# Optimization experiments

Hardware: AMD Instinct MI355X
Metric: run time of the kernel (lower is better)

## Reference

```python
import jax, jax.numpy as jnp
import numpy as np


def setup_inputs() -> dict:
    key = jax.random.key(0)
    k1, k2, k3 = jax.random.split(key, 3)
    B, L, S, H, E, D = 2, 512, 512, 8, 32, 64
    queries = jax.random.normal(k1, (B, L, H, E), dtype=jnp.float32)
    keys = jax.random.normal(k2, (B, S, H, E), dtype=jnp.float32)
    values = jax.random.normal(k3, (B, S, H, D), dtype=jnp.float32)
    v = jnp.ones((E,), dtype=jnp.float32)
    attn_mask_add = jnp.zeros((L, S), dtype=jnp.float32)
    key_lengths_add = jnp.zeros((B, S), dtype=jnp.float32)
    return {
        "queries": queries,
        "keys": keys,
        "values": values,
        "v": v,
        "attn_mask_add": attn_mask_add,
        "key_lengths_add": key_lengths_add,
    }


def reference(queries, keys, values, v, attn_mask_add, key_lengths_add):
    # Additive (Bahdanau) attention.
    # queries: (B,L,H,E), keys: (B,S,H,E), values: (B,S,H,D)
    # Broadcast add -> tanh -> contract with v: (B,L,S,H,E) -> (B,H,L,S)
    feat = jnp.tanh(queries[:, :, None, :, :] + keys[:, None, :, :, :])  # (B,L,S,H,E)
    scores = jnp.einsum("blshe,e->bhls", feat, v)  # (B,H,L,S)
    scores = scores + attn_mask_add[None, None, :, :]          # (L,S) attn mask
    scores = scores + key_lengths_add[:, None, None, :]        # (B,S) key-length mask
    A = jax.nn.softmax(scores, axis=-1)  # (B,H,L,S); dropout is identity (p=0 / eval)
    V = jnp.einsum("bhls,bshd->blhd", A, values)  # (B,L,H,D)
    return V
```

## Files before the change

kernel.cpp:

```cpp
#include <hip/hip_runtime.h>


#define BB 2
#define LL 512
#define SS 512
#define HH 8
#define EE 32
#define DD 64
#define TS 128
#define SASTR (SS + 8)

typedef __attribute__((ext_vector_type(8))) short bf16x8;
typedef __attribute__((ext_vector_type(4))) float f32x4;

__device__ __forceinline__ short f2bf(float f) {
    unsigned u = __float_as_uint(f);
    u += 0x7FFFu + ((u >> 16) & 1u);
    return (short)(u >> 16);
}

__device__ __forceinline__ float fast_exp2(float x) {
#if __has_builtin(__builtin_amdgcn_exp2f)
    return __builtin_amdgcn_exp2f(x);
#else
    return exp2f(x);
#endif
}
__device__ __forceinline__ float fast_rcp(float x) {
    return __builtin_amdgcn_rcpf(x);
}

__global__ __launch_bounds__(256) void addattn_kernel(
    const float* __restrict__ q,
    const float* __restrict__ k,
    const float* __restrict__ vals,
    const float* __restrict__ vvec,
    const float* __restrict__ mask,
    const float* __restrict__ klen,
    float* __restrict__ out)
{
    __shared__ float4 sk[EE / 4][TS];
    __shared__ short  sAb[4][SASTR];

    const int tid  = threadIdx.x;
    const int w    = tid >> 6;
    const int lane = tid & 63;
    const int bh   = blockIdx.x >> 7;
    const int lblk = blockIdx.x & 127;
    const int b    = bh >> 3;
    const int h    = bh & 7;
    const int l    = lblk * 4 + w;

    const float SC = 2.885390081777927f;

    float4 eq[EE / 4];
    {
        const float4* qrow = (const float4*)(q + (((size_t)b * LL + l) * HH + h) * EE);
        #pragma unroll
        for (int e4 = 0; e4 < EE / 4; e4++) {
            float4 t = qrow[e4];
            eq[e4] = make_float4(fast_exp2(SC * t.x), fast_exp2(SC * t.y),
                                 fast_exp2(SC * t.z), fast_exp2(SC * t.w));
        }
    }
    float4 v2[EE / 4];
    {
        const float4* vr = (const float4*)vvec;
        #pragma unroll
        for (int i = 0; i < EE / 4; i++) {
            float4 t = vr[i];
            v2[i] = make_float4(-2.f * t.x, -2.f * t.y, -2.f * t.z, -2.f * t.w);
        }
    }

    float sc[SS / 64];
    const float4* krow = (const float4*)(k + ((size_t)b * SS * HH + h) * EE);
    for (int t = 0; t < SS / TS; t++) {
        __syncthreads();
        #pragma unroll
        for (int i = 0; i < (TS * (EE / 4)) / 256; i++) {
            int idx = tid + i * 256;
            int ss  = idx >> 3;
            int e4  = idx & 7;
            float4 kv = krow[(size_t)(t * TS + ss) * (HH * EE / 4) + e4];
            sk[e4][ss ^ e4] = make_float4(
                fast_exp2(SC * kv.x), fast_exp2(SC * kv.y),
                fast_exp2(SC * kv.z), fast_exp2(SC * kv.w));
        }
        __syncthreads();
        #pragma unroll
        for (int j = 0; j < 2; j++) {
            int ssl = lane + j * 64;
            float a0 = 0.f, a1 = 0.f, a2 = 0.f, a3 = 0.f;
            #pragma unroll
            for (int e4 = 0; e4 < EE / 4; e4++) {
                float4 kv = sk[e4][ssl ^ e4];
                float4 ev = eq[e4];
                float4 vv = v2[e4];
                a0 = __builtin_fmaf(vv.x, fast_rcp(__builtin_fmaf(ev.x, kv.x, 1.f)), a0);
                a1 = __builtin_fmaf(vv.y, fast_rcp(__builtin_fmaf(ev.y, kv.y, 1.f)), a1);
                a2 = __builtin_fmaf(vv.z, fast_rcp(__builtin_fmaf(ev.z, kv.z, 1.f)), a2);
                a3 = __builtin_fmaf(vv.w, fast_rcp(__builtin_fmaf(ev.w, kv.w, 1.f)), a3);
            }
            sc[t * 2 + j] = (a0 + a1) + (a2 + a3);
        }
    }

    {
        const float* mrow = mask + (size_t)l * SS;
        const float* kl   = klen + (size_t)b * SS;
        float mx = -1e30f;
        #pragma unroll
        for (int i = 0; i < SS / 64; i++) {
            int s = lane + i * 64;
            sc[i] += mrow[s] + kl[s];
            mx = fmaxf(mx, sc[i]);
        }
        #pragma unroll
        for (int off = 1; off < 64; off <<= 1) mx = fmaxf(mx, __shfl_xor(mx, off, 64));
        float ssum = 0.f;
        #pragma unroll
        for (int i = 0; i < SS / 64; i++) {
            sc[i] = __expf(sc[i] - mx);
            ssum += sc[i];
        }
        #pragma unroll
        for (int off = 1; off < 64; off <<= 1) ssum += __shfl_xor(ssum, off, 64);
        float inv = fast_rcp(ssum);
        #pragma unroll
        for (int i = 0; i < SS / 64; i++)
            sAb[w][lane + i * 64] = f2bf(sc[i] * inv);
    }
    __syncthreads();

    const int am  = lane & 15;
    const int qd  = lane >> 4;
    const int dof = w * 16 + am;
    const float* vbase = vals + (((size_t)b * SS * HH + h) * DD) + dof;
    f32x4 acc = {0.f, 0.f, 0.f, 0.f};
    float vreg[8];
    #pragma unroll
    for (int j = 0; j < 8; j++)
        vreg[j] = vbase[(size_t)(qd * 8 + j) * (HH * DD)];
    for (int c = 0; c < SS / 32; c++) {
        bf16x8 bv;
        #pragma unroll
        for (int j = 0; j < 8; j++) bv[j] = f2bf(vreg[j]);
        if (c < SS / 32 - 1) {
            int s0n = (c + 1) * 32 + qd * 8;
            #pragma unroll
            for (int j = 0; j < 8; j++)
                vreg[j] = vbase[(size_t)(s0n + j) * (HH * DD)];
        }
        bf16x8 af = {0, 0, 0, 0, 0, 0, 0, 0};
        if (am < 4) af = *(const bf16x8*)&sAb[am][c * 32 + qd * 8];
        acc = __builtin_amdgcn_mfma_f32_16x16x32_bf16(af, bv, acc, 0, 0, 0);
    }
    if (qd == 0) {
        float* orow = out + (((size_t)b * LL + lblk * 4) * HH + h) * DD + dof;
        #pragma unroll
        for (int r = 0; r < 4; r++)
            orow[(size_t)r * (HH * DD)] = acc[r];
    }
}

extern "C" void kernel_launch(void* const* d_in, const int* in_sizes, int n_in,
                              void* d_out, int out_size, void* d_ws, size_t ws_size,
                              hipStream_t stream) {
    const float* q    = (const float*)d_in[0];
    const float* k    = (const float*)d_in[1];
    const float* vals = (const float*)d_in[2];
    const float* vvec = (const float*)d_in[3];
    const float* mask = (const float*)d_in[4];
    const float* klen = (const float*)d_in[5];
    float* outp = (float*)d_out;

    dim3 grid(BB * HH * (LL / 4));
    dim3 block(256);
    addattn_kernel<<<grid, block, 0, stream>>>(q, k, vals, vvec, mask, klen, outp);
}
```

Before: 106.4 us.

## Precompute exp(q), exp(k) tiles and transposed bf16 V in a prep kernel

Adds a prep kernel that computes exp2-scaled queries and keys, storing keys already in the swizzled tile layout, and packs values into a transposed bf16 buffer in workspace. The main kernel then copies key tiles straight into shared memory without recomputing exps, and loads 8 contiguous bf16 V elements per MFMA step instead of 8 strided fp32 loads plus conversion. The per-block redundant exp work on keys (repeated across 128 L-blocks) is removed, at the cost of an extra launch and a workspace round-trip. A leftover stub kernel that is never launched is also added.

```diff
diff --git a/kernel.cpp b/kernel.cpp
--- a/kernel.cpp
+++ b/kernel.cpp
@@ -8,17 +8,19 @@
 #define EE 32
 #define DD 64
 #define TS 128
-#define SASTR (SS + 8)
+
+#define WS_EK_OFF 0
+#define WS_EQ_OFF (2u * 1024u * 1024u)
+#define WS_VT_OFF (4u * 1024u * 1024u)
 
 typedef __attribute__((ext_vector_type(8))) short bf16x8;
 typedef __attribute__((ext_vector_type(4))) float f32x4;
 
-__device__ __forceinline__ short f2bf(float f) {
+__device__ __forceinline__ unsigned short f2bf(float f) {
     unsigned u = __float_as_uint(f);
     u += 0x7FFFu + ((u >> 16) & 1u);
-    return (short)(u >> 16);
-}
-
+    return (unsigned short)(u >> 16);
+}
 __device__ __forceinline__ float fast_exp2(float x) {
 #if __has_builtin(__builtin_amdgcn_exp2f)
     return __builtin_amdgcn_exp2f(x);
@@ -30,17 +32,56 @@
     return __builtin_amdgcn_rcpf(x);
 }
 
+#define SCV 2.885390081777927f
+
+__global__ __launch_bounds__(256) void prep_kernel(
+    const float* __restrict__ q, const float* __restrict__ k,
+    const float* __restrict__ vals, float* __restrict__ ws)
+{
+    unsigned gid = blockIdx.x * 256 + threadIdx.x;
+    if (gid < 65536u) {
+        unsigned i  = gid;
+        unsigned u  = i & 127u;
+        unsigned e4 = (i >> 7) & 7u;
+        unsigned t  = (i >> 10) & 3u;
+        unsigned h  = (i >> 12) & 7u;
+        unsigned b  = i >> 15;
+        unsigned s  = t * 128u + (u ^ e4);
+        float4 kv = *(const float4*)(k + (((size_t)b * SS + s) * HH + h) * EE + e4 * 4);
+        float4 ev = make_float4(fast_exp2(SCV * kv.x), fast_exp2(SCV * kv.y),
+                                fast_exp2(SCV * kv.z), fast_exp2(SCV * kv.w));
+        ((float4*)(ws + WS_EK_OFF / 4))[i] = ev;
+    } else if (gid < 131072u) {
+        unsigned i = gid - 65536u;
+        float4 qv = ((const float4*)q)[i];
+        float4 ev = make_float4(fast_exp2(SCV * qv.x), fast_exp2(SCV * qv.y),
+                                fast_exp2(SCV * qv.z), fast_exp2(SCV * qv.w));
+        ((float4*)(ws + WS_EQ_OFF / 4))[i] = ev;
+    } else {
+        unsigned p  = gid - 131072u;
+        unsigned d  = p & 63u;
+        unsigned sp = (p >> 6) & 255u;
+        unsigned h  = (p >> 14) & 7u;
+        unsigned b  = p >> 17;
+        unsigned s0 = sp * 2u;
+        float f0 = vals[(((size_t)b * SS + s0) * HH + h) * DD + d];
+        float f1 = vals[(((size_t)b * SS + s0 + 1) * HH + h) * DD + d];
+        unsigned pk = (unsigned)f2bf(f0) | ((unsigned)f2bf(f1) << 16);
+        unsigned* vt = (unsigned*)((char*)ws + WS_VT_OFF);
+        vt[(((size_t)b * HH + h) * DD + d) * (SS / 2) + sp] = pk;
+    }
+}
+
 __global__ __launch_bounds__(256) void addattn_kernel(
-    const float* __restrict__ q,
-    const float* __restrict__ k,
-    const float* __restrict__ vals,
-    const float* __restrict__ vvec,
+    const float* __restrict__ ws_ekf,
+    const float* __restrict__ ws_eqf,
+    const unsigned short* __restrict__ ws_vt,
     const float* __restrict__ mask,
     const float* __restrict__ klen,
     float* __restrict__ out)
 {
     __shared__ float4 sk[EE / 4][TS];
-    __shared__ short  sAb[4][SASTR];
+    __shared__ short  sAb[4][SS];
 
     const int tid  = threadIdx.x;
     const int w    = tid >> 6;
@@ -51,17 +92,49 @@
     const int h    = bh & 7;
     const int l    = lblk * 4 + w;
 
-    const float SC = 2.885390081777927f;
-
     float4 eq[EE / 4];
     {
-        const float4* qrow = (const float4*)(q + (((size_t)b * LL + l) * HH + h) * EE);
-        #pragma unroll
-        for (int e4 = 0; e4 < EE / 4; e4++) {
-            float4 t = qrow[e4];
-            eq[e4] = make_float4(fast_exp2(SC * t.x), fast_exp2(SC * t.y),
-                                 fast_exp2(SC * t.z), fast_exp2(SC * t.w));
-        }
+        const float4* qrow =
+            (const float4*)(ws_eqf + (((size_t)b * LL + l) * HH + h) * EE);
+        #pragma unroll
+        for (int e4 = 0; e4 < EE / 4; e4++) eq[e4] = qrow[e4];
+    }
+    float4 v2[EE / 4];
+    {
+    }
+    (void)v2;
+
+    (void)sk; (void)sAb; (void)eq; (void)ws_vt; (void)mask; (void)klen;
+    (void)out; (void)lane; (void)b; (void)h; (void)l;
+}
+
+__global__ __launch_bounds__(256) void addattn2_kernel(
+    const float* __restrict__ ws_ekf,
+    const float* __restrict__ ws_eqf,
+    const unsigned short* __restrict__ ws_vt,
+    const float* __restrict__ vvec,
+    const float* __restrict__ mask,
+    const float* __restrict__ klen,
+    float* __restrict__ out)
+{
+    __shared__ float4 sk[EE / 4][TS];
+    __shared__ short  sAb[4][SS];
+
+    const int tid  = threadIdx.x;
+    const int w    = tid >> 6;
+    const int lane = tid & 63;
+    const int bh   = blockIdx.x >> 7;
+    const int lblk = blockIdx.x & 127;
+    const int b    = bh >> 3;
+    const int h    = bh & 7;
+    const int l    = lblk * 4 + w;
+
+    float4 eq[EE / 4];
+    {
+        const float4* qrow =
+            (const float4*)(ws_eqf + (((size_t)b * LL + l) * HH + h) * EE);
+        #pragma unroll
+        for (int e4 = 0; e4 < EE / 4; e4++) eq[e4] = qrow[e4];
     }
     float4 v2[EE / 4];
     {
@@ -74,19 +147,15 @@
     }
 
     float sc[SS / 64];
-    const float4* krow = (const float4*)(k + ((size_t)b * SS * HH + h) * EE);
+    const float4* ektiles =
+        (const float4*)ws_ekf + ((size_t)(b * HH + h) * 4) * (8 * TS);
+    float4* skl = &sk[0][0];
     for (int t = 0; t < SS / TS; t++) {
         __syncthreads();
-        #pragma unroll
-        for (int i = 0; i < (TS * (EE / 4)) / 256; i++) {
-            int idx = tid + i * 256;
-            int ss  = idx >> 3;
-            int e4  = idx & 7;
-            float4 kv = krow[(size_t)(t * TS + ss) * (HH * EE / 4) + e4];
-            sk[e4][ss ^ e4] = make_float4(
-                fast_exp2(SC * kv.x), fast_exp2(SC * kv.y),
-                fast_exp2(SC * kv.z), fast_exp2(SC * kv.w));
-        }
+        const float4* src = ektiles + (size_t)t * (8 * TS);
+        #pragma unroll
+        for (int i = 0; i < 4; i++)
+            skl[tid + i * 256] = src[tid + i * 256];
         __syncthreads();
         #pragma unroll
         for (int j = 0; j < 2; j++) {
@@ -129,32 +198,24 @@
         float inv = fast_rcp(ssum);
         #pragma unroll
         for (int i = 0; i < SS / 64; i++)
-            sAb[w][lane + i * 64] = f2bf(sc[i] * inv);
+            sAb[w][lane + i * 64] = (short)f2bf(sc[i] * inv);
     }
     __syncthreads();
 
     const int am  = lane & 15;
     const int qd  = lane >> 4;
     const int dof = w * 16 + am;
-    const float* vbase = vals + (((size_t)b * SS * HH + h) * DD) + dof;
+    const unsigned short* vt =
+        ws_vt + (((size_t)b * HH + h) * DD + dof) * SS + qd * 8;
     f32x4 acc = {0.f, 0.f, 0.f, 0.f};
-    float vreg[8];
-    #pragma unroll
-    for (int j = 0; j < 8; j++)
-        vreg[j] = vbase[(size_t)(qd * 8 + j) * (HH * DD)];
+    bf16x8 bcur = *(const bf16x8*)vt;
     for (int c = 0; c < SS / 32; c++) {
-        bf16x8 bv;
-        #pragma unroll
-        for (int j = 0; j < 8; j++) bv[j] = f2bf(vreg[j]);
-        if (c < SS / 32 - 1) {
-            int s0n = (c + 1) * 32 + qd * 8;
-            #pragma unroll
-            for (int j = 0; j < 8; j++)
-                vreg[j] = vbase[(size_t)(s0n + j) * (HH * DD)];
-        }
+        bf16x8 bnxt = bcur;
+        if (c < SS / 32 - 1) bnxt = *(const bf16x8*)(vt + (c + 1) * 32);
         bf16x8 af = {0, 0, 0, 0, 0, 0, 0, 0};
         if (am < 4) af = *(const bf16x8*)&sAb[am][c * 32 + qd * 8];
-        acc = __builtin_amdgcn_mfma_f32_16x16x32_bf16(af, bv, acc, 0, 0, 0);
+        acc = __builtin_amdgcn_mfma_f32_16x16x32_bf16(af, bcur, acc, 0, 0, 0);
+        bcur = bnxt;
     }
     if (qd == 0) {
         float* orow = out + (((size_t)b * LL + lblk * 4) * HH + h) * DD + dof;
@@ -175,7 +236,12 @@
     const float* klen = (const float*)d_in[5];
     float* outp = (float*)d_out;
 
-    dim3 grid(BB * HH * (LL / 4));
-    dim3 block(256);
-    addattn_kernel<<<grid, block, 0, stream>>>(q, k, vals, vvec, mask, klen, outp);
-}
+    float* ws = (float*)d_ws;
+    prep_kernel<<<dim3(1536), dim3(256), 0, stream>>>(q, k, vals, ws);
+
+    const float* ws_ekf = (const float*)((char*)d_ws + WS_EK_OFF);
+    const float* ws_eqf = (const float*)((char*)d_ws + WS_EQ_OFF);
+    const unsigned short* ws_vt = (const unsigned short*)((char*)d_ws + WS_VT_OFF);
+    addattn2_kernel<<<dim3(BB * HH * (LL / 4)), dim3(256), 0, stream>>>(
+        ws_ekf, ws_eqf, ws_vt, vvec, mask, klen, outp);
+}
```

Result: no change. 108.0 us (+1.4%).
